# Kernel tuning notes

Measured on AMD Instinct MI355X. Metric: run time of the kernel, lower is better.

The kernel has to match this reference:

```python
import jax, jax.numpy as jnp
import numpy as np

NUM_GROUPS = 8
NUM_HEADS = 8
EPS = 1e-5


def setup_inputs() -> dict:
    key = jax.random.key(0)
    k1, k2, k3 = jax.random.split(key, 3)
    b, c, h, w = 16, 512, 32, 32
    x = jax.random.normal(k1, (b, c, h, w), dtype=jnp.float32)
    gn_w = jnp.ones((c,), dtype=jnp.float32)
    gn_b = jnp.zeros((c,), dtype=jnp.float32)
    qkv_w = jax.random.normal(k2, (3 * c, c), dtype=jnp.float32) * (1.0 / np.sqrt(c))
    qkv_b = jnp.zeros((3 * c,), dtype=jnp.float32)
    proj_w = jax.random.normal(k3, (c, c), dtype=jnp.float32) * (1.0 / np.sqrt(c))
    proj_b = jnp.zeros((c,), dtype=jnp.float32)
    return {"x": x, "gn_w": gn_w, "gn_b": gn_b, "qkv_w": qkv_w,
            "qkv_b": qkv_b, "proj_w": proj_w, "proj_b": proj_b}


def reference(x, gn_w, gn_b, qkv_w, qkv_b, proj_w, proj_b):
    b, c, h, w = x.shape
    H = NUM_HEADS
    d = c // H
    N = h * w
    scale = d ** (-0.5)

    # GroupNorm(8, c), affine
    xg = x.reshape(b, NUM_GROUPS, -1)
    mu = xg.mean(axis=-1, keepdims=True)
    var = xg.var(axis=-1, keepdims=True)
    xn = ((xg - mu) * jax.lax.rsqrt(var + EPS)).reshape(b, c, h, w)
    xn = xn * gn_w[None, :, None, None] + gn_b[None, :, None, None]

    # 1x1 conv qkv: [b, 3c, h, w]
    qkv = jnp.einsum('oc,bchw->bohw', qkv_w, xn) + qkv_b[None, :, None, None]
    # 'b (three h d) x y -> three b h (x y) d'
    qkv = qkv.reshape(b, 3, H, d, N)          # (b, 3, H, d, N)
    q = jnp.swapaxes(qkv[:, 0], -1, -2)       # (b, H, N, d)
    k = jnp.swapaxes(qkv[:, 1], -1, -2)
    v = jnp.swapaxes(qkv[:, 2], -1, -2)

    attn = jnp.einsum('bhid,bhjd->bhij', q, k) * scale
    attn = jax.nn.softmax(attn, axis=-1)
    out = jnp.einsum('bhij,bhjd->bhid', attn, v)  # (b, H, N, d)

    # 'b h (x y) d -> b (h d) x y'
    out = jnp.swapaxes(out, -1, -2).reshape(b, c, h, w)
    out = jnp.einsum('oc,bchw->bohw', proj_w, out) + proj_b[None, :, None, None]
    return x + out
```

## Files before the change

kernel.cpp:

```cpp
#include <hip/hip_runtime.h>
#include <math.h>

typedef unsigned short u16;
typedef __attribute__((ext_vector_type(8))) short short8;
typedef __attribute__((ext_vector_type(4))) float floatx4;
typedef __attribute__((ext_vector_type(4))) u16 v4u16;
typedef __attribute__((ext_vector_type(8))) u16 v8u16;

#define B_   16
#define C_   512
#define NSP  1024
#define EPSV 1e-5f
#define QSCALE 0.18033688011117f

__device__ __forceinline__ u16 f2bf(float f) {
  union { float f; unsigned u; } v; v.f = f;
  unsigned r = v.u + 0x7FFFu + ((v.u >> 16) & 1u);
  return (u16)(r >> 16);
}

__device__ __forceinline__ void gld16(const u16* g, u16* l) {
  __builtin_amdgcn_global_load_lds(
      (const __attribute__((address_space(1))) void*)g,
      (__attribute__((address_space(3))) void*)l, 16, 0, 0);
}

__device__ __forceinline__ short8 lds_read_b128(const u16* p) {
  short8 r;
  asm volatile("ds_read_b128 %0, %1"
               : "=&v"(r)
               : "v"((const __attribute__((address_space(3))) u16*)p));
  return r;
}

__device__ __forceinline__ unsigned pk_bf(float a, float b) {
  return __builtin_amdgcn_perm(__float_as_uint(b), __float_as_uint(a), 0x07060302u);
}

__global__ __launch_bounds__(256) void gn_stats_cvt(
    const float* __restrict__ x, float* __restrict__ stats,
    const float* __restrict__ qa, u16* __restrict__ oa,
    const float* __restrict__ pa, u16* __restrict__ ob)
{
  int blk = blockIdx.x;
  if (blk >= 1024) {
    int cb = blk - 1024;
    const float* in; u16* out; int i;
    if (cb < 768) { in = qa; out = oa; i = (cb * 256 + threadIdx.x) * 4; }
    else          { in = pa; out = ob; i = ((cb - 768) * 256 + threadIdx.x) * 4; }
    float4 v = *(const float4*)(in + i);
    v4u16 o = { f2bf(v.x), f2bf(v.y), f2bf(v.z), f2bf(v.w) };
    *(v4u16*)(out + i) = o;
    return;
  }
  int bg = blk >> 3, ck = blk & 7;
  const float4* xp = (const float4*)(x + (((size_t)bg * 64 + ck * 8) * NSP));
  float s = 0.f, ss = 0.f;
#pragma unroll
  for (int it = 0; it < 8; ++it) {
    float4 v = xp[it * 256 + threadIdx.x];
    s  += v.x + v.y + v.z + v.w;
    ss += v.x * v.x + v.y * v.y + v.z * v.z + v.w * v.w;
  }
  for (int off = 32; off > 0; off >>= 1) {
    s  += __shfl_down(s, off);
    ss += __shfl_down(ss, off);
  }
  __shared__ float rs[4], rss[4];
  int lane = threadIdx.x & 63, wv = threadIdx.x >> 6;
  if (lane == 0) { rs[wv] = s; rss[wv] = ss; }
  __syncthreads();
  if (threadIdx.x == 0) {
    float S  = rs[0] + rs[1] + rs[2] + rs[3];
    float SS = rss[0] + rss[1] + rss[2] + rss[3];
    atomicAdd(&stats[bg * 2], S);
    atomicAdd(&stats[bg * 2 + 1], SS);
  }
}

__global__ __launch_bounds__(256) void gn_apply(
    const float* __restrict__ x, const float* __restrict__ stats,
    const float* __restrict__ gw, const float* __restrict__ gb,
    u16* __restrict__ xn)
{
  int blk = blockIdx.x;
  int bg = blk >> 4, nt = blk & 15;
  int b = bg >> 3, g = bg & 7;
  float S = stats[bg * 2], SS = stats[bg * 2 + 1];
  float mu  = S * (1.f / 65536.f);
  float var = SS * (1.f / 65536.f) - mu * mu;
  float inv = rsqrtf(var + EPSV);
  __shared__ float T[64][65];
  const float* xb = x + (size_t)bg * 64 * NSP;
  int t = threadIdx.x;
#pragma unroll
  for (int it = 0; it < 4; ++it) {
    int task = it * 256 + t;
    int cc = task >> 4, ns = task & 15;
    float4 v = *(const float4*)(xb + (size_t)cc * NSP + nt * 64 + ns * 4);
    T[cc][ns * 4 + 0] = v.x; T[cc][ns * 4 + 1] = v.y;
    T[cc][ns * 4 + 2] = v.z; T[cc][ns * 4 + 3] = v.w;
  }
  __syncthreads();
#pragma unroll
  for (int it = 0; it < 2; ++it) {
    int task = it * 256 + t;
    int n = task >> 3, cs = task & 7;
    v8u16 o;
#pragma unroll
    for (int u = 0; u < 8; ++u) {
      int cg = g * 64 + cs * 8 + u;
      float val = (T[cs * 8 + u][n] - mu) * inv * gw[cg] + gb[cg];
      o[u] = f2bf(val);
    }
    *(v8u16*)(xn + ((size_t)b * NSP + nt * 64 + n) * C_ + g * 64 + cs * 8) = o;
  }
}

template <int MODE>
__global__ __launch_bounds__(256) void gemm_mfma(
    const u16* __restrict__ W, const u16* __restrict__ X,
    const float* __restrict__ bias, const float* __restrict__ resid,
    u16* __restrict__ out_qk, u16* __restrict__ out_v,
    float* __restrict__ out_f)
{
  __shared__ u16 smem[24576];
  int id = blockIdx.x;
  int yb = id >> 7, rr = id & 127;
  int b = rr >> 3, xb_ = rr & 7;
  int m0 = yb * 128, n0 = xb_ * 128;
  int t = threadIdx.x, lane = t & 63, w = t >> 6;
  int c = lane & 15, q = lane >> 4;
  int wm = w >> 1, wn = w & 1;
  const u16* Xb = X + (size_t)b * NSP * C_;

  floatx4 acc[4][4];
#pragma unroll
  for (int mi = 0; mi < 4; ++mi)
#pragma unroll
    for (int ni = 0; ni < 4; ++ni) acc[mi][ni] = (floatx4){0.f, 0.f, 0.f, 0.f};

  auto stage = [&](int buf, int k0) {
    u16* Asb = smem + buf * 8192;
    u16* Bsb = Asb + 4096;
#pragma unroll
    for (int it = 0; it < 2; ++it) {
      int task = it * 256 + t;
      int mr = task >> 2;
      int gk = (task & 3) ^ ((mr >> 1) & 3);
      gld16(W + (size_t)(m0 + mr) * C_ + k0 + gk * 8, Asb + task * 8);
    }
#pragma unroll
    for (int it = 0; it < 2; ++it) {
      int task = it * 256 + t;
      int nr = task >> 2;
      int gk = (task & 3) ^ ((nr >> 1) & 3);
      gld16(Xb + (size_t)(n0 + nr) * C_ + k0 + gk * 8, Bsb + task * 8);
    }
  };

  auto compute = [&](int buf) {
    const u16* As = smem + buf * 8192;
    const u16* Bs = As + 4096;
    short8 af[4], bfr[4];
#pragma unroll
    for (int mi = 0; mi < 4; ++mi) {
      int m = wm * 64 + mi * 16 + c;
      af[mi] = lds_read_b128(As + m * 32 + ((q ^ ((m >> 1) & 3)) << 3));
    }
#pragma unroll
    for (int ni = 0; ni < 4; ++ni) {
      int n = wn * 64 + ni * 16 + c;
      bfr[ni] = lds_read_b128(Bs + n * 32 + ((q ^ ((n >> 1) & 3)) << 3));
    }
    asm volatile("s_waitcnt lgkmcnt(0)" ::: "memory");
    __builtin_amdgcn_sched_barrier(0);
#pragma unroll
    for (int mi = 0; mi < 4; ++mi)
#pragma unroll
      for (int ni = 0; ni < 4; ++ni)
        acc[mi][ni] = __builtin_amdgcn_mfma_f32_16x16x32_bf16(
            af[mi], bfr[ni], acc[mi][ni], 0, 0, 0);
  };

  stage(0, 0);
  stage(1, 32);
  int cur = 0, tgt = 2;
  for (int ki = 0; ki < 14; ++ki) {
    asm volatile("s_waitcnt vmcnt(4)" ::: "memory");
    __builtin_amdgcn_s_barrier();
    stage(tgt, (ki + 2) * 32);
    compute(cur);
    cur = (cur == 2) ? 0 : cur + 1;
    tgt = (tgt == 2) ? 0 : tgt + 1;
  }
  asm volatile("s_waitcnt vmcnt(4)" ::: "memory");
  __builtin_amdgcn_s_barrier();
  compute(2);
  asm volatile("s_waitcnt vmcnt(0)" ::: "memory");
  __builtin_amdgcn_s_barrier();
  compute(0);
  __syncthreads();

  if (MODE == 0) {
    if (m0 < 1024) {
      float sc = (m0 < 512) ? QSCALE : 1.0f;
      u16* Cl = smem;
#pragma unroll
      for (int mi = 0; mi < 4; ++mi) {
        floatx4 bi = *(const floatx4*)(bias + m0 + wm * 64 + mi * 16 + q * 4);
#pragma unroll
        for (int ni = 0; ni < 4; ++ni) {
          int n = wn * 64 + ni * 16 + c;
          int m = wm * 64 + mi * 16 + q * 4;
          v4u16 pk;
#pragma unroll
          for (int r = 0; r < 4; ++r) pk[r] = f2bf((acc[mi][ni][r] + bi[r]) * sc);
          *(v4u16*)(Cl + n * 136 + m) = pk;
        }
      }
      __syncthreads();
#pragma unroll
      for (int it = 0; it < 8; ++it) {
        int task = it * 256 + t;
        int n = task >> 4, seg = task & 15;
        v8u16 v = *(const v8u16*)(Cl + n * 136 + seg * 8);
        *(v8u16*)(out_qk + ((size_t)b * NSP + n0 + n) * 1024 + m0 + seg * 8) = v;
      }
    } else {
      u16* Cl = smem;
#pragma unroll
      for (int mi = 0; mi < 4; ++mi) {
        floatx4 bi = *(const floatx4*)(bias + m0 + wm * 64 + mi * 16 + q * 4);
#pragma unroll
        for (int ni = 0; ni < 4; ++ni) {
          int n = wn * 64 + ni * 16 + c;
          int m = wm * 64 + mi * 16 + q * 4;
#pragma unroll
          for (int r = 0; r < 4; ++r)
            Cl[(m + r) * 136 + n] = f2bf(acc[mi][ni][r] + bi[r]);
        }
      }
      __syncthreads();
#pragma unroll
      for (int it = 0; it < 8; ++it) {
        int task = it * 256 + t;
        int m = task >> 4, seg = task & 15;
        int g64 = seg >> 3, s = seg & 7;
        int k0 = ((s & 4) << 3) | ((s & 1) << 4) | ((s & 2) << 1);
        v8u16 v = *(const v8u16*)(Cl + m * 136 + seg * 8);
        v4u16 lo = { v[0], v[1], v[2], v[3] };
        v4u16 hi = { v[4], v[5], v[6], v[7] };
        size_t base = ((size_t)b * C_ + m0 - 1024 + m) * NSP + n0 + g64 * 64;
        *(v4u16*)(out_v + base + k0) = lo;
        *(v4u16*)(out_v + base + k0 + 8) = hi;
      }
    }
  } else {
#pragma unroll
    for (int mi = 0; mi < 4; ++mi) {
      floatx4 bi = *(const floatx4*)(bias + m0 + wm * 64 + mi * 16 + q * 4);
#pragma unroll
      for (int ni = 0; ni < 4; ++ni) {
        int n = n0 + wn * 64 + ni * 16 + c;
        int m = m0 + wm * 64 + mi * 16 + q * 4;
#pragma unroll
        for (int r = 0; r < 4; ++r) {
          size_t o = ((size_t)b * C_ + m + r) * NSP + n;
          out_f[o] = acc[mi][ni][r] + bi[r] + resid[o];
        }
      }
    }
  }
}

__global__ __launch_bounds__(256, 4) void attn_mfma(
    const u16* __restrict__ qk, const u16* __restrict__ vbuf,
    u16* __restrict__ att)
{
  __shared__ u16 __align__(16) smem[16384];
  int id = blockIdx.x;
  int hb = id & 127;
  int i0 = id >> 7;
  int h = hb >> 4, b = hb & 15;
  int t = threadIdx.x, lane = t & 63, w = t >> 6;
  int c = lane & 15, q = lane >> 4;
  const u16* qbase = qk + (size_t)b * NSP * 1024;
  const u16* vbase = vbuf + (size_t)(b * C_ + h * 64) * NSP;

#pragma unroll
  for (int it = 0; it < 4; ++it) {
    int task = it * 256 + t;
    int r = task >> 3, seg = task & 7, ds = (seg ^ (r & 7)) * 8;
    gld16(qbase + (size_t)(i0 * 128 + r) * 1024 + h * 64 + ds, smem + task * 8);
  }
#pragma unroll
  for (int it = 0; it < 2; ++it) {
    int task = it * 256 + t;
    int r = task >> 3, seg = task & 7, ds = (seg ^ (r & 7)) * 8;
    gld16(qbase + (size_t)r * 1024 + 512 + h * 64 + ds, smem + 8192 + task * 8);
    gld16(vbase + (size_t)r * NSP + ds, smem + 12288 + task * 8);
  }
  __syncthreads();

  short8 qa[2][2];
#pragma unroll
  for (int nf = 0; nf < 2; ++nf) {
    int row = w * 32 + nf * 16 + c;
#pragma unroll
    for (int ch = 0; ch < 2; ++ch)
      qa[nf][ch] = *(const short8*)(smem + row * 64 + (((q + 4 * ch) ^ (c & 7)) << 3));
  }
  __syncthreads();

  short8 onesf;
#pragma unroll
  for (int u = 0; u < 8; ++u) onesf[u] = (short)0x3F80;

  floatx4 Oacc[4][2];
  floatx4 OaccT[2];
#pragma unroll
  for (int dt = 0; dt < 4; ++dt)
#pragma unroll
    for (int nf = 0; nf < 2; ++nf) Oacc[dt][nf] = (floatx4){0.f, 0.f, 0.f, 0.f};
#pragma unroll
  for (int nf = 0; nf < 2; ++nf) OaccT[nf] = (floatx4){0.f, 0.f, 0.f, 0.f};

  for (int j0 = 0; j0 < 16; ++j0) {
    int p = j0 & 1;
    u16* KS = smem + (p ? 0 : 8192);
    u16* VS = KS + 4096;
    if (j0 < 15) {
      u16* KN = smem + (p ? 8192 : 0);
      u16* VN = KN + 4096;
#pragma unroll
      for (int it = 0; it < 2; ++it) {
        int task = it * 256 + t;
        int r = task >> 3, seg = task & 7, ds = (seg ^ (r & 7)) * 8;
        gld16(qbase + (size_t)((j0 + 1) * 64 + r) * 1024 + 512 + h * 64 + ds,
              KN + task * 8);
        gld16(vbase + (size_t)r * NSP + (j0 + 1) * 64 + ds, VN + task * 8);
      }
      asm volatile("s_waitcnt vmcnt(4)" ::: "memory");
    } else {
      asm volatile("s_waitcnt vmcnt(0)" ::: "memory");
    }
    __builtin_amdgcn_sched_barrier(0);
#pragma unroll
    for (int jt2 = 0; jt2 < 2; ++jt2) {
      short8 kb[2][2], vf[4];
#pragma unroll
      for (int jj = 0; jj < 2; ++jj) {
        int row = (jt2 * 2 + jj) * 16 + c;
        kb[jj][0] = lds_read_b128(KS + row * 64 + ((q ^ (row & 7)) << 3));
        kb[jj][1] = lds_read_b128(KS + row * 64 + (((q + 4) ^ (row & 7)) << 3));
      }
#pragma unroll
      for (int dt = 0; dt < 4; ++dt) {
        int dd = dt * 16 + c;
        vf[dt] = lds_read_b128(VS + dd * 64 + (((jt2 * 4 + q) ^ (dd & 7)) << 3));
      }
      asm volatile("s_waitcnt lgkmcnt(0)" ::: "memory");
      __builtin_amdgcn_sched_barrier(0);
      unsigned pk2[2][2][2];
#pragma unroll
      for (int jj = 0; jj < 2; ++jj) {
#pragma unroll
        for (int nf = 0; nf < 2; ++nf) {
          floatx4 z = (floatx4){0.f, 0.f, 0.f, 0.f};
          z = __builtin_amdgcn_mfma_f32_16x16x32_bf16(kb[jj][0], qa[nf][0], z, 0, 0, 0);
          z = __builtin_amdgcn_mfma_f32_16x16x32_bf16(kb[jj][1], qa[nf][1], z, 0, 0, 0);
          float p0 = __builtin_amdgcn_exp2f(z[0]);
          float p1 = __builtin_amdgcn_exp2f(z[1]);
          float p2 = __builtin_amdgcn_exp2f(z[2]);
          float p3 = __builtin_amdgcn_exp2f(z[3]);
          pk2[jj][nf][0] = pk_bf(p0, p1);
          pk2[jj][nf][1] = pk_bf(p2, p3);
        }
      }
      short8 pf[2];
#pragma unroll
      for (int nf = 0; nf < 2; ++nf) {
        union { short8 s; unsigned d[4]; } u;
        u.d[0] = pk2[0][nf][0]; u.d[1] = pk2[0][nf][1];
        u.d[2] = pk2[1][nf][0]; u.d[3] = pk2[1][nf][1];
        pf[nf] = u.s;
      }
      __builtin_amdgcn_s_setprio(1);
#pragma unroll
      for (int dt = 0; dt < 4; ++dt)
#pragma unroll
        for (int nf = 0; nf < 2; ++nf)
          Oacc[dt][nf] = __builtin_amdgcn_mfma_f32_16x16x32_bf16(
              vf[dt], pf[nf], Oacc[dt][nf], 0, 0, 0);
#pragma unroll
      for (int nf = 0; nf < 2; ++nf)
        OaccT[nf] = __builtin_amdgcn_mfma_f32_16x16x32_bf16(
            onesf, pf[nf], OaccT[nf], 0, 0, 0);
      __builtin_amdgcn_s_setprio(0);
    }
    __builtin_amdgcn_s_barrier();
  }

#pragma unroll
  for (int nf = 0; nf < 2; ++nf) {
    float rinv = 1.f / OaccT[nf][0];
    int n = i0 * 128 + w * 32 + nf * 16 + c;
#pragma unroll
    for (int dt = 0; dt < 4; ++dt) {
      v4u16 pk;
#pragma unroll
      for (int r = 0; r < 4; ++r) pk[r] = f2bf(Oacc[dt][nf][r] * rinv);
      *(v4u16*)(att + ((size_t)b * NSP + n) * C_ + h * 64 + dt * 16 + q * 4) = pk;
    }
  }
}

extern "C" void kernel_launch(void* const* d_in, const int* in_sizes, int n_in,
                              void* d_out, int out_size, void* d_ws, size_t ws_size,
                              hipStream_t stream)
{
  const float* x    = (const float*)d_in[0];
  const float* gw   = (const float*)d_in[1];
  const float* gb   = (const float*)d_in[2];
  const float* qkvw = (const float*)d_in[3];
  const float* qkvb = (const float*)d_in[4];
  const float* pw   = (const float*)d_in[5];
  const float* pb   = (const float*)d_in[6];
  float* out = (float*)d_out;

  u16* xn    = (u16*)d_ws;
  u16* qkb   = xn   + 8388608;
  u16* vbf   = qkb  + 16777216;
  u16* attb  = vbf  + 8388608;
  u16* wq    = attb + 8388608;
  u16* wp    = wq   + 786432;
  float* stats = (float*)(wp + 262144);

  hipMemsetAsync(stats, 0, 128 * 2 * sizeof(float), stream);
  gn_stats_cvt<<<2048, 256, 0, stream>>>(x, stats, qkvw, wq, pw, wp);
  gn_apply<<<2048, 256, 0, stream>>>(x, stats, gw, gb, xn);
  gemm_mfma<0><<<dim3(1536), 256, 0, stream>>>(
      wq, xn, qkvb, nullptr, qkb, vbf, nullptr);
  attn_mfma<<<dim3(1024), 256, 0, stream>>>(qkb, vbf, attb);
  gemm_mfma<1><<<dim3(512), 256, 0, stream>>>(
      wp, attb, pb, x, nullptr, nullptr, out);
}
```

Baseline: 193.0 us.

## Load GEMM weight fragments directly to registers, halving LDS footprint

The GEMM kernel no longer stages the weight tile through LDS. Each wave loads its A fragments straight from global memory into registers with double-buffered dwordx4 loads, and only the activation tile goes through the three-stage LDS ring. This halves shared memory per block to allow more resident blocks and removes the A-side LDS reads. The epilogue is split into two halves so it fits the smaller buffer, which adds extra barriers and makes weight rows be fetched redundantly by the two wn waves.

```diff
diff --git a/kernel.cpp b/kernel.cpp
--- a/kernel.cpp
+++ b/kernel.cpp
@@ -31,6 +31,22 @@
                : "=&v"(r)
                : "v"((const __attribute__((address_space(3))) u16*)p));
   return r;
+}
+
+__device__ __forceinline__ short8 gload_b128(const u16* p) {
+  short8 r;
+  asm volatile("global_load_dwordx4 %0, %1, off"
+               : "=&v"(r)
+               : "v"((const __attribute__((address_space(1))) u16*)p)
+               : "memory");
+  return r;
+}
+
+template <int N> __device__ __forceinline__ void wait_vm() {
+  asm volatile("s_waitcnt vmcnt(%0)" :: "n"(N) : "memory");
+}
+template <int N> __device__ __forceinline__ void wait_vm_lgkm() {
+  asm volatile("s_waitcnt vmcnt(%0) lgkmcnt(0)" :: "n"(N) : "memory");
 }
 
 __device__ __forceinline__ unsigned pk_bf(float a, float b) {
@@ -124,7 +140,7 @@
     u16* __restrict__ out_qk, u16* __restrict__ out_v,
     float* __restrict__ out_f)
 {
-  __shared__ u16 smem[24576];
+  __shared__ u16 smem[12288];
   int id = blockIdx.x;
   int yb = id >> 7, rr = id & 127;
   int b = rr >> 3, xb_ = rr & 7;
@@ -140,16 +156,8 @@
 #pragma unroll
     for (int ni = 0; ni < 4; ++ni) acc[mi][ni] = (floatx4){0.f, 0.f, 0.f, 0.f};
 
-  auto stage = [&](int buf, int k0) {
-    u16* Asb = smem + buf * 8192;
-    u16* Bsb = Asb + 4096;
-#pragma unroll
-    for (int it = 0; it < 2; ++it) {
-      int task = it * 256 + t;
-      int mr = task >> 2;
-      int gk = (task & 3) ^ ((mr >> 1) & 3);
-      gld16(W + (size_t)(m0 + mr) * C_ + k0 + gk * 8, Asb + task * 8);
-    }
+  auto stageB = [&](int buf, int k0) {
+    u16* Bsb = smem + buf * 4096;
 #pragma unroll
     for (int it = 0; it < 2; ++it) {
       int task = it * 256 + t;
@@ -159,47 +167,57 @@
     }
   };
 
-  auto compute = [&](int buf) {
-    const u16* As = smem + buf * 8192;
-    const u16* Bs = As + 4096;
-    short8 af[4], bfr[4];
-#pragma unroll
-    for (int mi = 0; mi < 4; ++mi) {
-      int m = wm * 64 + mi * 16 + c;
-      af[mi] = lds_read_b128(As + m * 32 + ((q ^ ((m >> 1) & 3)) << 3));
-    }
-#pragma unroll
-    for (int ni = 0; ni < 4; ++ni) {
-      int n = wn * 64 + ni * 16 + c;
-      bfr[ni] = lds_read_b128(Bs + n * 32 + ((q ^ ((n >> 1) & 3)) << 3));
-    }
-    asm volatile("s_waitcnt lgkmcnt(0)" ::: "memory");
-    __builtin_amdgcn_sched_barrier(0);
-#pragma unroll
-    for (int mi = 0; mi < 4; ++mi)
-#pragma unroll
-      for (int ni = 0; ni < 4; ++ni)
-        acc[mi][ni] = __builtin_amdgcn_mfma_f32_16x16x32_bf16(
-            af[mi], bfr[ni], acc[mi][ni], 0, 0, 0);
-  };
-
-  stage(0, 0);
-  stage(1, 32);
-  int cur = 0, tgt = 2;
-  for (int ki = 0; ki < 14; ++ki) {
-    asm volatile("s_waitcnt vmcnt(4)" ::: "memory");
-    __builtin_amdgcn_s_barrier();
-    stage(tgt, (ki + 2) * 32);
-    compute(cur);
-    cur = (cur == 2) ? 0 : cur + 1;
-    tgt = (tgt == 2) ? 0 : tgt + 1;
-  }
-  asm volatile("s_waitcnt vmcnt(4)" ::: "memory");
-  __builtin_amdgcn_s_barrier();
-  compute(2);
-  asm volatile("s_waitcnt vmcnt(0)" ::: "memory");
-  __builtin_amdgcn_s_barrier();
-  compute(0);
+  const u16* wl[4];
+#pragma unroll
+  for (int mi = 0; mi < 4; ++mi)
+    wl[mi] = W + (size_t)(m0 + wm * 64 + mi * 16 + c) * C_ + q * 8;
+
+  short8 afA[4], afB[4];
+
+  stageB(0, 0);
+  stageB(1, 32);
+#pragma unroll
+  for (int mi = 0; mi < 4; ++mi) afA[mi] = gload_b128(wl[mi]);
+
+#define GEMM_BODY(KI, AFC, AFN, BUFC, DOSTAGE, DOAF, PREW, MFW)            \
+  {                                                                        \
+    if (PREW) wait_vm<4>();      \
+    __builtin_amdgcn_s_barrier();                                          \
+    if (DOSTAGE) stageB(((BUFC) + 2) % 3, ((KI) + 2) * 32);                \
+    if (DOAF) {                                                            \
+      _Pragma("unroll")                                                    \
+      for (int mi = 0; mi < 4; ++mi)                                       \
+        AFN[mi] = gload_b128(wl[mi] + ((KI) + 1) * 32);                    \
+    }                                                                      \
+    __builtin_amdgcn_sched_barrier(0);                                     \
+    const u16* Bs = smem + (BUFC) * 4096;                                  \
+    short8 bfr[4];                                                         \
+    _Pragma("unroll")                                                      \
+    for (int ni = 0; ni < 4; ++ni) {                                       \
+      int n = wn * 64 + ni * 16 + c;                                       \
+      bfr[ni] = lds_read_b128(Bs + n * 32 + ((q ^ ((n >> 1) & 3)) << 3));  \
+    }                                                                      \
+    wait_vm_lgkm<MFW>();                                                   \
+    __builtin_amdgcn_sched_barrier(0);                                     \
+    _Pragma("unroll")                                                      \
+    for (int mi = 0; mi < 4; ++mi) {                                       \
+      _Pragma("unroll")                                                    \
+      for (int ni = 0; ni < 4; ++ni)                                       \
+        acc[mi][ni] = __builtin_amdgcn_mfma_f32_16x16x32_bf16(             \
+            AFC[mi], bfr[ni], acc[mi][ni], 0, 0, 0);                       \
+    }                                                                      \
+  }
+
+  GEMM_BODY(0, afA, afB, 0, true, true, true, 6);
+  GEMM_BODY(1, afB, afA, 1, true, true, false, 6);
+#pragma unroll
+  for (int kk = 1; kk <= 6; ++kk) {
+    GEMM_BODY(2 * kk,     afA, afB, (2 * kk) % 3,     true, true, false, 6);
+    GEMM_BODY(2 * kk + 1, afB, afA, (2 * kk + 1) % 3, true, true, false, 6);
+  }
+  GEMM_BODY(14, afA, afB, 2, false, true,  false, 4);
+  GEMM_BODY(15, afB, afA, 0, false, false, false, 0);
+#undef GEMM_BODY
   __syncthreads();
 
   if (MODE == 0) {
@@ -207,53 +225,67 @@
       float sc = (m0 < 512) ? QSCALE : 1.0f;
       u16* Cl = smem;
 #pragma unroll
-      for (int mi = 0; mi < 4; ++mi) {
-        floatx4 bi = *(const floatx4*)(bias + m0 + wm * 64 + mi * 16 + q * 4);
-#pragma unroll
-        for (int ni = 0; ni < 4; ++ni) {
-          int n = wn * 64 + ni * 16 + c;
-          int m = wm * 64 + mi * 16 + q * 4;
-          v4u16 pk;
-#pragma unroll
-          for (int r = 0; r < 4; ++r) pk[r] = f2bf((acc[mi][ni][r] + bi[r]) * sc);
-          *(v4u16*)(Cl + n * 136 + m) = pk;
-        }
-      }
-      __syncthreads();
-#pragma unroll
-      for (int it = 0; it < 8; ++it) {
-        int task = it * 256 + t;
-        int n = task >> 4, seg = task & 15;
-        v8u16 v = *(const v8u16*)(Cl + n * 136 + seg * 8);
-        *(v8u16*)(out_qk + ((size_t)b * NSP + n0 + n) * 1024 + m0 + seg * 8) = v;
+      for (int mh = 0; mh < 2; ++mh) {
+        if (wm == mh) {
+#pragma unroll
+          for (int mi = 0; mi < 4; ++mi) {
+            floatx4 bi = *(const floatx4*)(bias + m0 + mh * 64 + mi * 16 + q * 4);
+#pragma unroll
+            for (int ni = 0; ni < 4; ++ni) {
+              int n = wn * 64 + ni * 16 + c;
+              int ml = mi * 16 + q * 4;
+              v4u16 pk;
+#pragma unroll
+              for (int r = 0; r < 4; ++r) pk[r] = f2bf((acc[mi][ni][r] + bi[r]) * sc);
+              *(v4u16*)(Cl + n * 72 + ml) = pk;
+            }
+          }
+        }
+        __syncthreads();
+#pragma unroll
+        for (int it = 0; it < 4; ++it) {
+          int task = it * 256 + t;
+          int n = task >> 3, seg = task & 7;
+          v8u16 v = *(const v8u16*)(Cl + n * 72 + seg * 8);
+          *(v8u16*)(out_qk + ((size_t)b * NSP + n0 + n) * 1024 +
+                    m0 + mh * 64 + seg * 8) = v;
+        }
+        __syncthreads();
       }
     } else {
       u16* Cl = smem;
 #pragma unroll
-      for (int mi = 0; mi < 4; ++mi) {
-        floatx4 bi = *(const floatx4*)(bias + m0 + wm * 64 + mi * 16 + q * 4);
-#pragma unroll
-        for (int ni = 0; ni < 4; ++ni) {
-          int n = wn * 64 + ni * 16 + c;
-          int m = wm * 64 + mi * 16 + q * 4;
-#pragma unroll
-          for (int r = 0; r < 4; ++r)
-            Cl[(m + r) * 136 + n] = f2bf(acc[mi][ni][r] + bi[r]);
-        }
-      }
-      __syncthreads();
-#pragma unroll
-      for (int it = 0; it < 8; ++it) {
-        int task = it * 256 + t;
-        int m = task >> 4, seg = task & 15;
-        int g64 = seg >> 3, s = seg & 7;
-        int k0 = ((s & 4) << 3) | ((s & 1) << 4) | ((s & 2) << 1);
-        v8u16 v = *(const v8u16*)(Cl + m * 136 + seg * 8);
-        v4u16 lo = { v[0], v[1], v[2], v[3] };
-        v4u16 hi = { v[4], v[5], v[6], v[7] };
-        size_t base = ((size_t)b * C_ + m0 - 1024 + m) * NSP + n0 + g64 * 64;
-        *(v4u16*)(out_v + base + k0) = lo;
-        *(v4u16*)(out_v + base + k0 + 8) = hi;
+      for (int mh = 0; mh < 2; ++mh) {
+        if (wm == mh) {
+#pragma unroll
+          for (int mi = 0; mi < 4; ++mi) {
+            floatx4 bi = *(const floatx4*)(bias + m0 + mh * 64 + mi * 16 + q * 4);
+#pragma unroll
+            for (int ni = 0; ni < 4; ++ni) {
+              int n = wn * 64 + ni * 16 + c;
+              int ml = mi * 16 + q * 4;
+#pragma unroll
+              for (int r = 0; r < 4; ++r)
+                Cl[(ml + r) * 136 + n] = f2bf(acc[mi][ni][r] + bi[r]);
+            }
+          }
+        }
+        __syncthreads();
+#pragma unroll
+        for (int it = 0; it < 4; ++it) {
+          int task = it * 256 + t;
+          int m = task >> 4, seg = task & 15;
+          int g64 = seg >> 3, s = seg & 7;
+          int k0 = ((s & 4) << 3) | ((s & 1) << 4) | ((s & 2) << 1);
+          v8u16 v = *(const v8u16*)(Cl + m * 136 + seg * 8);
+          v4u16 lo = { v[0], v[1], v[2], v[3] };
+          v4u16 hi = { v[4], v[5], v[6], v[7] };
+          size_t base = ((size_t)b * C_ + m0 - 1024 + mh * 64 + m) * NSP +
+                        n0 + g64 * 64;
+          *(v4u16*)(out_v + base + k0) = lo;
+          *(v4u16*)(out_v + base + k0 + 8) = hi;
+        }
+        __syncthreads();
       }
     }
   } else {
```

Result: slower. 224.1 us (+16.1%).
